# Optimization experiments

Hardware: AMD Instinct MI355X
Metric: run time of the kernel (lower is better)

The kernel has to match this reference:

```python
import jax, jax.numpy as jnp
import numpy as np


def _silu(x):
    return x * jax.nn.sigmoid(x)


def setup_inputs() -> dict:
    key = jax.random.key(0)
    ks = jax.random.split(key, 5)
    B, N, H, D = 4, 2048, 4, 64
    T = B * N
    q = jax.random.normal(ks[0], (T, H, D), jnp.float32)
    k = jax.random.normal(ks[1], (T, H, D), jnp.float32)
    v = jax.random.normal(ks[2], (T, H, D), jnp.float32)
    g_cmp = jax.random.uniform(ks[3], (T, H, 1), jnp.float32)
    g_slc = jax.random.uniform(ks[4], (T, H, 1), jnp.float32)
    x_offsets = jnp.arange(B + 1, dtype=jnp.int32) * N  # equal-length jagged offsets
    return {"q": q, "k": k, "v": v, "g_cmp": g_cmp, "g_slc": g_slc, "x_offsets": x_offsets}


def reference(q, k, v, g_cmp, g_slc, x_offsets, block_size=32, block_counts=4):
    T, H, D = q.shape
    B = int(x_offsets.shape[0]) - 1
    N = T // B                      # equal-length sequences (offsets = arange*N)
    BS = block_size
    Nb = N // BS                    # compressed blocks per sequence
    scale = float(D) ** -0.5

    qb = q.reshape(B, N, H, D)
    kb = k.reshape(B, N, H, D)
    vb = v.reshape(B, N, H, D)

    # --- compressed branch: per-block mean pooling of K/V (index_add / counts) ---
    k_cmp = kb.reshape(B, Nb, BS, H, D).mean(axis=2)   # [B,Nb,H,D]
    v_cmp = vb.reshape(B, Nb, BS, H, D).mean(axis=2)

    scores = jnp.einsum('bnhd,bmhd->bhnm', qb, k_cmp) * scale  # [B,H,N,Nb]
    blk_q = jnp.arange(N) // BS
    causal_cmp = blk_q[:, None] >= jnp.arange(Nb)[None, :]      # [N,Nb]
    p_cmp = jnp.where(causal_cmp[None, None], _silu(scores), 0.0)
    o_cmp = jnp.einsum('bhnm,bmhd->bnhd', p_cmp, v_cmp)
    o_cmp = o_cmp * g_cmp.reshape(B, N, H)[..., None]

    # --- block selection: per-(query,head) top-S compressed blocks ---
    masked = jnp.where(causal_cmp[None, None], scores, -jnp.inf)
    S = min(block_counts, Nb)
    _, topk = jax.lax.top_k(masked, S)                          # [B,H,N,S]

    # --- selected branch: gather S blocks of raw K/V per query, SiLU attention ---
    qh = qb.transpose(0, 2, 1, 3)  # [B,H,N,D]
    kh = kb.transpose(0, 2, 1, 3)
    vh = vb.transpose(0, 2, 1, 3)
    bi = jnp.arange(B)[:, None, None, None]
    hi = jnp.arange(H)[None, :, None, None]
    pos_q = jnp.arange(N)
    acc = jnp.zeros((B, H, N, D), q.dtype)
    for s in range(S):  # small static loop over selected blocks
        b_idx = topk[..., s]                                    # [B,H,N]
        pos = b_idx[..., None] * BS + jnp.arange(BS)            # [B,H,N,BS] local key pos
        kg = kh[bi, hi, pos]                                    # [B,H,N,BS,D]
        vg = vh[bi, hi, pos]
        sc = jnp.einsum('bhnd,bhnkd->bhnk', qh, kg) * scale
        caus = pos <= pos_q[None, None, :, None]                # strict per-token causal
        p = jnp.where(caus, _silu(sc), 0.0)
        acc = acc + jnp.einsum('bhnk,bhnkd->bhnd', p, vg)
    o_slc = acc.transpose(0, 2, 1, 3) * g_slc.reshape(B, N, H)[..., None]

    return o_cmp.reshape(T, H, D), o_slc.reshape(T, H, D)
```

## Files before the change

kernel.cpp:

```cpp
#include <hip/hip_runtime.h>
#include <math.h>

#define BB   4
#define NSEQ 2048
#define HH_  4
#define DD   64
#define BS   32
#define NB   (NSEQ/BS)
#define SSEL 4
#define SCALE 0.125f
#define WPB  8

__device__ __forceinline__ float silu_f(float x) {
    return x / (1.0f + __expf(-x));
}

__device__ __forceinline__ float RL(float x, int lane_lit) {
    return __int_as_float(__builtin_amdgcn_readlane(__float_as_int(x), lane_lit));
}

template<bool KT>
__global__ __launch_bounds__(256) void pool_kernel(
    const float* __restrict__ k, const float* __restrict__ v,
    float* __restrict__ kc4, float* __restrict__ vcmp, float* __restrict__ kT4)
{
    __shared__ float s_part[2][4][DD];
    int wg = blockIdx.x;
    int h = wg % HH_;
    int m = (wg / HH_) % NB;
    int b = wg / (HH_ * NB);
    int wave = threadIdx.x >> 6;
    int lane = threadIdx.x & 63;

    int row0 = m * BS + wave * 8;
    const float* kbase = k + ((size_t)(b * NSEQ + row0) * HH_ + h) * DD + lane;
    const float* vbase = v + ((size_t)(b * NSEQ + row0) * HH_ + h) * DD + lane;
    float* kTb = KT ? kT4 + (((size_t)(b * HH_ + h) * (DD / 4) + (lane >> 2)) * NSEQ
                              + row0) * 4 + (lane & 3)
                    : nullptr;
    float ks = 0.f, vs = 0.f;
    #pragma unroll
    for (int j = 0; j < 8; ++j) {
        float kv = kbase[(size_t)j * HH_ * DD];
        ks += kv;
        if (KT) kTb[(size_t)j * 4] = kv;
        vs += vbase[(size_t)j * HH_ * DD];
    }
    s_part[0][wave][lane] = ks;
    s_part[1][wave][lane] = vs;
    __syncthreads();
    if (wave == 0) {
        float kst = (s_part[0][0][lane] + s_part[0][1][lane]
                   + s_part[0][2][lane] + s_part[0][3][lane]) * (1.0f / BS);
        float vst = (s_part[1][0][lane] + s_part[1][1][lane]
                   + s_part[1][2][lane] + s_part[1][3][lane]) * (1.0f / BS);
        kc4[(((size_t)(b * HH_ + h) * (DD / 4) + (lane >> 2)) * NB + m) * 4 + (lane & 3)] = kst;
        vcmp[(((size_t)(b * NB + m) * HH_ + h) * DD) + lane] = vst;
    }
}

template<bool KT>
__global__ __launch_bounds__(512) void bsa_kernel(
    const float* __restrict__ q, const float* __restrict__ k, const float* __restrict__ v,
    const float* __restrict__ g_cmp, const float* __restrict__ g_slc,
    const float* __restrict__ kc4, const float* __restrict__ vcmp,
    const float* __restrict__ kT4,
    float* __restrict__ o_cmp, float* __restrict__ o_slc)
{
    __shared__ float4 s_kc4[(DD / 4) * NB];
    __shared__ float  s_vc [NB * DD];

    int tid = threadIdx.x;
    int bh  = (blockIdx.x * WPB) / NSEQ;
    int h   = bh % HH_;
    int b   = bh / HH_;

    const float4* kc4g = reinterpret_cast<const float4*>(kc4) + (size_t)bh * (DD / 4) * NB;
    #pragma unroll
    for (int i = 0; i < 2; ++i)
        s_kc4[tid + 512 * i] = kc4g[tid + 512 * i];
    const float* vp0 = vcmp + ((size_t)(b * NB) * HH_ + h) * DD;
    #pragma unroll
    for (int i = 0; i < 2; ++i) {
        int idx = tid + 512 * i;
        reinterpret_cast<float4*>(s_vc)[idx] =
            *reinterpret_cast<const float4*>(vp0 + (size_t)(idx >> 4) * HH_ * DD + (idx & 15) * 4);
    }
    __syncthreads();

    int lane = tid & 63;
    int gw = blockIdx.x * WPB + (tid >> 6);
    int n  = gw % NSEQ;
    int blk_q = n >> 5;

    size_t qoff = ((size_t)(b * NSEQ + n) * HH_ + h) * DD;
    float q_l = q[qoff + lane] * SCALE;

    float sc = 0.f;
    #pragma unroll
    for (int d4 = 0; d4 < DD / 4; ++d4) {
        float4 kk = s_kc4[d4 * NB + lane];
        sc += RL(q_l, 4 * d4 + 0) * kk.x
            + RL(q_l, 4 * d4 + 1) * kk.y
            + RL(q_l, 4 * d4 + 2) * kk.z
            + RL(q_l, 4 * d4 + 3) * kk.w;
    }
    bool valid = (lane <= blk_q);
    float p = valid ? silu_f(sc) : 0.f;

    float acc = 0.f;
    #pragma unroll
    for (int c = 0; c < 4; ++c) {
        if (c * 16 <= blk_q) {
            #pragma unroll
            for (int mm = 0; mm < 16; ++mm) {
                int m = c * 16 + mm;
                acc += RL(p, m) * s_vc[m * DD + lane];
            }
        }
    }
    float g1 = g_cmp[(size_t)(b * NSEQ + n) * HH_ + h];
    o_cmp[qoff + lane] = acc * g1;

    float tv = valid ? sc : -INFINITY;
    int myidx = lane;
    int sel[SSEL];
    #pragma unroll
    for (int s = 0; s < SSEL; ++s) {
        float bv = tv; int bi = myidx;
        #pragma unroll
        for (int off = 32; off >= 1; off >>= 1) {
            float ov = __shfl_xor(bv, off);
            int   oi = __shfl_xor(bi, off);
            if (ov > bv || (ov == bv && oi < bi)) { bv = ov; bi = oi; }
        }
        sel[s] = bi & 63;
        if (myidx == bi) { tv = -INFINITY; myidx = lane + 64; }
    }

    int j = lane & 31;
    int half = lane >> 5;
    float accs = 0.f;
    #pragma unroll
    for (int sp = 0; sp < SSEL / 2; ++sp) {
        int bs0 = sel[2 * sp];
        int bs1 = sel[2 * sp + 1];
        if (bs0 > blk_q && bs1 > blk_q) continue;
        int bsme = half ? bs1 : bs0;
        int pos = bsme * BS + j;
        float dot = 0.f;
        if (KT) {
            const float4* kTb = reinterpret_cast<const float4*>(kT4)
                              + (size_t)bh * (DD / 4) * NSEQ + pos;
            #pragma unroll
            for (int t4 = 0; t4 < DD / 4; ++t4) {
                float4 kk = kTb[(size_t)t4 * NSEQ];
                dot += RL(q_l, 4 * t4 + 0) * kk.x
                     + RL(q_l, 4 * t4 + 1) * kk.y
                     + RL(q_l, 4 * t4 + 2) * kk.z
                     + RL(q_l, 4 * t4 + 3) * kk.w;
            }
        } else {
            const float* krow = k + ((size_t)(b * NSEQ + pos) * HH_ + h) * DD;
            #pragma unroll
            for (int t4 = 0; t4 < DD / 4; ++t4) {
                float4 kk = *reinterpret_cast<const float4*>(krow + 4 * t4);
                dot += RL(q_l, 4 * t4 + 0) * kk.x
                     + RL(q_l, 4 * t4 + 1) * kk.y
                     + RL(q_l, 4 * t4 + 2) * kk.z
                     + RL(q_l, 4 * t4 + 3) * kk.w;
            }
        }
        float pj = (pos <= n) ? silu_f(dot) : 0.f;

        const float* vb0 = v + ((size_t)(b * NSEQ + bs0 * BS) * HH_ + h) * DD + lane;
        const float* vb1 = v + ((size_t)(b * NSEQ + bs1 * BS) * HH_ + h) * DD + lane;
        #pragma unroll
        for (int jj = 0; jj < BS; ++jj) {
            accs += RL(pj, jj)      * vb0[(size_t)jj * HH_ * DD];
            accs += RL(pj, 32 + jj) * vb1[(size_t)jj * HH_ * DD];
        }
    }
    float g2 = g_slc[(size_t)(b * NSEQ + n) * HH_ + h];
    o_slc[qoff + lane] = accs * g2;
}

extern "C" void kernel_launch(void* const* d_in, const int* in_sizes, int n_in,
                              void* d_out, int out_size, void* d_ws, size_t ws_size,
                              hipStream_t stream) {
    const float* q     = (const float*)d_in[0];
    const float* k     = (const float*)d_in[1];
    const float* v     = (const float*)d_in[2];
    const float* g_cmp = (const float*)d_in[3];
    const float* g_slc = (const float*)d_in[4];

    const size_t THD = (size_t)BB * NSEQ * HH_ * DD;
    float* o_cmp = (float*)d_out;
    float* o_slc = (float*)d_out + THD;

    const size_t CSZ = (size_t)BB * HH_ * DD * NB;
    float* kc4  = (float*)d_ws;
    float* vcmp = (float*)d_ws + CSZ;
    float* kT4  = (float*)d_ws + 2 * CSZ;
    const size_t need_bytes = (2 * CSZ + THD) * sizeof(float);

    int pool_wgs = BB * NB * HH_;
    int bsa_wgs  = (BB * NSEQ * HH_) / WPB;

    if (ws_size >= need_bytes) {
        pool_kernel<true><<<pool_wgs, 256, 0, stream>>>(k, v, kc4, vcmp, kT4);
        bsa_kernel<true><<<bsa_wgs, 512, 0, stream>>>(q, k, v, g_cmp, g_slc,
                                                      kc4, vcmp, kT4, o_cmp, o_slc);
    } else {
        pool_kernel<false><<<pool_wgs, 256, 0, stream>>>(k, v, kc4, vcmp, nullptr);
        bsa_kernel<false><<<bsa_wgs, 512, 0, stream>>>(q, k, v, g_cmp, g_slc,
                                                       kc4, vcmp, nullptr, o_cmp, o_slc);
    }
}
```

Baseline: 164.7 us.

## Use scalar q loads, fold scale into pooled keys, split PV across lane groups

Result: slower. 202.7 us (+23.0%).

```diff
diff --git a/kernel.cpp b/kernel.cpp
--- a/kernel.cpp
+++ b/kernel.cpp
@@ -17,6 +17,13 @@
 
 __device__ __forceinline__ float RL(float x, int lane_lit) {
     return __int_as_float(__builtin_amdgcn_readlane(__float_as_int(x), lane_lit));
+}
+
+__device__ __forceinline__ const float* uniform_ptr(const float* p) {
+    uintptr_t a = (uintptr_t)p;
+    uint32_t lo = __builtin_amdgcn_readfirstlane((uint32_t)(a & 0xffffffffu));
+    uint32_t hi = __builtin_amdgcn_readfirstlane((uint32_t)(a >> 32));
+    return (const float*)((((uintptr_t)hi) << 32) | (uintptr_t)lo);
 }
 
 template<bool KT>
@@ -43,7 +50,7 @@
     for (int j = 0; j < 8; ++j) {
         float kv = kbase[(size_t)j * HH_ * DD];
         ks += kv;
-        if (KT) kTb[(size_t)j * 4] = kv;
+        if (KT) kTb[(size_t)j * 4] = kv * SCALE;
         vs += vbase[(size_t)j * HH_ * DD];
     }
     s_part[0][wave][lane] = ks;
@@ -51,7 +58,7 @@
     __syncthreads();
     if (wave == 0) {
         float kst = (s_part[0][0][lane] + s_part[0][1][lane]
-                   + s_part[0][2][lane] + s_part[0][3][lane]) * (1.0f / BS);
+                   + s_part[0][2][lane] + s_part[0][3][lane]) * (SCALE / BS);
         float vst = (s_part[1][0][lane] + s_part[1][1][lane]
                    + s_part[1][2][lane] + s_part[1][3][lane]) * (1.0f / BS);
         kc4[(((size_t)(b * HH_ + h) * (DD / 4) + (lane >> 2)) * NB + m) * 4 + (lane & 3)] = kst;
@@ -94,16 +101,14 @@
     int blk_q = n >> 5;
 
     size_t qoff = ((size_t)(b * NSEQ + n) * HH_ + h) * DD;
-    float q_l = q[qoff + lane] * SCALE;
+    const float* qrow = uniform_ptr(q + qoff);
 
     float sc = 0.f;
     #pragma unroll
     for (int d4 = 0; d4 < DD / 4; ++d4) {
         float4 kk = s_kc4[d4 * NB + lane];
-        sc += RL(q_l, 4 * d4 + 0) * kk.x
-            + RL(q_l, 4 * d4 + 1) * kk.y
-            + RL(q_l, 4 * d4 + 2) * kk.z
-            + RL(q_l, 4 * d4 + 3) * kk.w;
+        sc += qrow[4 * d4 + 0] * kk.x + qrow[4 * d4 + 1] * kk.y
+            + qrow[4 * d4 + 2] * kk.z + qrow[4 * d4 + 3] * kk.w;
     }
     bool valid = (lane <= blk_q);
     float p = valid ? silu_f(sc) : 0.f;
@@ -140,7 +145,9 @@
 
     int j = lane & 31;
     int half = lane >> 5;
-    float accs = 0.f;
+    int g  = lane >> 4;
+    int d4 = lane & 15;
+    float4 acc4 = {0.f, 0.f, 0.f, 0.f};
     #pragma unroll
     for (int sp = 0; sp < SSEL / 2; ++sp) {
         int bs0 = sel[2 * sp];
@@ -155,34 +162,42 @@
             #pragma unroll
             for (int t4 = 0; t4 < DD / 4; ++t4) {
                 float4 kk = kTb[(size_t)t4 * NSEQ];
-                dot += RL(q_l, 4 * t4 + 0) * kk.x
-                     + RL(q_l, 4 * t4 + 1) * kk.y
-                     + RL(q_l, 4 * t4 + 2) * kk.z
-                     + RL(q_l, 4 * t4 + 3) * kk.w;
+                dot += qrow[4 * t4 + 0] * kk.x + qrow[4 * t4 + 1] * kk.y
+                     + qrow[4 * t4 + 2] * kk.z + qrow[4 * t4 + 3] * kk.w;
             }
         } else {
             const float* krow = k + ((size_t)(b * NSEQ + pos) * HH_ + h) * DD;
             #pragma unroll
             for (int t4 = 0; t4 < DD / 4; ++t4) {
                 float4 kk = *reinterpret_cast<const float4*>(krow + 4 * t4);
-                dot += RL(q_l, 4 * t4 + 0) * kk.x
-                     + RL(q_l, 4 * t4 + 1) * kk.y
-                     + RL(q_l, 4 * t4 + 2) * kk.z
-                     + RL(q_l, 4 * t4 + 3) * kk.w;
+                dot += qrow[4 * t4 + 0] * kk.x + qrow[4 * t4 + 1] * kk.y
+                     + qrow[4 * t4 + 2] * kk.z + qrow[4 * t4 + 3] * kk.w;
             }
+            dot *= SCALE;
         }
         float pj = (pos <= n) ? silu_f(dot) : 0.f;
 
-        const float* vb0 = v + ((size_t)(b * NSEQ + bs0 * BS) * HH_ + h) * DD + lane;
-        const float* vb1 = v + ((size_t)(b * NSEQ + bs1 * BS) * HH_ + h) * DD + lane;
+        int bpv = (g >= 2) ? bs1 : bs0;
+        const float* vrow = v + ((size_t)(b * NSEQ + bpv * BS + (g & 1) * 16) * HH_ + h) * DD
+                          + d4 * 4;
         #pragma unroll
-        for (int jj = 0; jj < BS; ++jj) {
-            accs += RL(pj, jj)      * vb0[(size_t)jj * HH_ * DD];
-            accs += RL(pj, 32 + jj) * vb1[(size_t)jj * HH_ * DD];
-        }
-    }
+        for (int t = 0; t < 16; ++t) {
+            float pb = __shfl(pj, (lane & 48) + t);
+            float4 vv = *reinterpret_cast<const float4*>(vrow + (size_t)t * HH_ * DD);
+            acc4.x += pb * vv.x; acc4.y += pb * vv.y;
+            acc4.z += pb * vv.z; acc4.w += pb * vv.w;
+        }
+    }
+    acc4.x += __shfl_xor(acc4.x, 16); acc4.y += __shfl_xor(acc4.y, 16);
+    acc4.z += __shfl_xor(acc4.z, 16); acc4.w += __shfl_xor(acc4.w, 16);
+    acc4.x += __shfl_xor(acc4.x, 32); acc4.y += __shfl_xor(acc4.y, 32);
+    acc4.z += __shfl_xor(acc4.z, 32); acc4.w += __shfl_xor(acc4.w, 32);
     float g2 = g_slc[(size_t)(b * NSEQ + n) * HH_ + h];
-    o_slc[qoff + lane] = accs * g2;
+    if (lane < 16) {
+        float4 o;
+        o.x = acc4.x * g2; o.y = acc4.y * g2; o.z = acc4.z * g2; o.w = acc4.w * g2;
+        *reinterpret_cast<float4*>(&o_slc[qoff + lane * 4]) = o;
+    }
 }
 
 extern "C" void kernel_launch(void* const* d_in, const int* in_sizes, int n_in,
```
